# Optimization experiments

Measured on AMD Instinct MI355X. Metric: run time of the kernel, lower is better.

Reference implementation:

```python
import jax, jax.numpy as jnp
import numpy as np

H = 16        # head_nums
DN = 128      # qk_nope_head_dim
DR = 64       # qk_rope_head_dim
DV = 128      # v_head_dim
QLR = 1536    # q_lora_rank
KVLR = 512    # kv_lora_rank
HID = 2048    # hidden_dim
THETA = 10000.0
EPS = 1e-6


def _rms(x, w):
    return x * jax.lax.rsqrt(jnp.mean(x * x, axis=-1, keepdims=True) + EPS) * w


def _reorder(x):
    # replicates view(b,h,s,d//2,2).transpose(4,3).reshape: [x0,x2,...,x1,x3,...]
    return jnp.concatenate([x[..., 0::2], x[..., 1::2]], axis=-1)


def _rotate_half(x):
    h = x.shape[-1] // 2
    return jnp.concatenate([-x[..., h:], x[..., :h]], axis=-1)


def setup_inputs() -> dict:
    key = jax.random.key(0)
    ks = jax.random.split(key, 7)
    B, S = 1, 2048

    def w(k, i, o):
        return jax.random.normal(k, (i, o), jnp.float32) * (i ** -0.5)

    return {
        "x": jax.random.normal(ks[0], (B, S, HID), jnp.float32),
        "Wq_down": w(ks[1], HID, QLR),
        "q_norm_w": jnp.ones((QLR,), jnp.float32),
        "Wq_up": w(ks[2], QLR, H * (DN + DR)),
        "Wkv_down": w(ks[3], HID, KVLR + DR),
        "kv_norm_w": jnp.ones((KVLR,), jnp.float32),
        "Wkv_up": w(ks[4], KVLR, H * (DN + DV)),
        "Wo": w(ks[5], HID, HID),
        "position": jnp.broadcast_to(jnp.arange(S, dtype=jnp.int32)[None], (B, S)),
        "mask": jnp.tril(jnp.ones((S, S), bool))[None, None],  # causal [1,1,S,S]
    }


def reference(x, Wq_down, q_norm_w, Wq_up, Wkv_down, kv_norm_w, Wkv_up, Wo, position, mask):
    B, S, _ = x.shape
    # low-rank Q path: down-proj -> RMSNorm -> up-proj -> [B,H,S,DN+DR]
    q = _rms(x @ Wq_down, q_norm_w) @ Wq_up
    q = q.reshape(B, S, H, DN + DR).transpose(0, 2, 1, 3)
    q_nope, q_rope = q[..., :DN], q[..., DN:]
    # latent KV path
    ckv = x @ Wkv_down
    c, k_rope = ckv[..., :KVLR], ckv[..., KVLR:]
    c = _rms(c, kv_norm_w)
    kv = (c @ Wkv_up).reshape(B, S, H, DN + DV).transpose(0, 2, 1, 3)
    k_nope, v = kv[..., :DN], kv[..., DN:]
    k_rope = k_rope[:, None]  # [B,1,S,DR] shared across heads
    # rotary tables
    inv_freq = 1.0 / (THETA ** (jnp.arange(0, DR, 2, dtype=jnp.float32) / DR))
    t = jnp.arange(S, dtype=jnp.float32)
    emb = jnp.concatenate([jnp.outer(t, inv_freq)] * 2, axis=-1)  # [S,DR]
    cos = jnp.cos(emb)[position][:, None]  # [B,1,S,DR]
    sin = jnp.sin(emb)[position][:, None]
    qr, kr = _reorder(q_rope), _reorder(k_rope)
    q_rot = qr * cos + _rotate_half(qr) * sin
    k_rot = kr * cos + _rotate_half(kr) * sin
    q_state = jnp.concatenate([q_nope, q_rot], axis=-1)              # [B,H,S,DN+DR]
    k_state = jnp.concatenate(
        [k_nope, jnp.broadcast_to(k_rot, (B, H, S, DR))], axis=-1)   # [B,H,S,DN+DR]
    scores = jnp.einsum('bhsd,bhtd->bhst', q_state, k_state) / np.float32(np.sqrt(DV))
    scores = jnp.where(mask, scores, -jnp.inf)
    att = jax.nn.softmax(scores, axis=-1)
    out = jnp.einsum('bhst,bhtd->bhsd', att, v)
    out = out.transpose(0, 2, 1, 3).reshape(B, S, H * DV)
    return out @ Wo
```

## Files before the change

kernel.cpp:

```cpp
#include <hip/hip_runtime.h>
#include <hip/hip_bf16.h>
#include <cstddef>

#define H 16
#define DN 128
#define DR 64
#define DV 128
#define QLR 1536
#define KVLR 512
#define HID 2048
#define SLEN 2048
#define EPS 1e-6f
#define SCALE 0.08838834764831845f
#define QK_SCALE (0.08838834764831845f * 1.4426950408889634f)

typedef __attribute__((ext_vector_type(8))) short short8;
typedef __attribute__((ext_vector_type(4))) float f32x4;
typedef unsigned short u16;

__device__ __forceinline__ u16 f2bf(float f) {
    __hip_bfloat16 h = __float2bfloat16(f);
    return __builtin_bit_cast(u16, h);
}
__device__ __forceinline__ float b2f(u16 v) {
    return __bfloat162float(__builtin_bit_cast(__hip_bfloat16, v));
}
__device__ __forceinline__ unsigned pack2(float a, float b) {
    return (unsigned)f2bf(a) | ((unsigned)f2bf(b) << 16);
}

__global__ __launch_bounds__(256) void prep_all(
    const float* __restrict__ x, u16* __restrict__ xb,
    const float* __restrict__ Wqd, const float* __restrict__ Wkvd,
    const float* __restrict__ Wqu, const float* __restrict__ Wkvu,
    const float* __restrict__ Wo,
    u16* __restrict__ BtF, u16* __restrict__ Wqu_t,
    u16* __restrict__ Wkvu_t, u16* __restrict__ Wo_t)
{
    const int tid = threadIdx.x;
    if (blockIdx.x < 2048) {
        size_t base = ((size_t)blockIdx.x * 256 + tid) * 8;
        float4 v0 = *reinterpret_cast<const float4*>(x + base);
        float4 v1 = *reinterpret_cast<const float4*>(x + base + 4);
        union { short8 s; unsigned u[4]; } p;
        p.u[0] = pack2(v0.x, v0.y); p.u[1] = pack2(v0.z, v0.w);
        p.u[2] = pack2(v1.x, v1.y); p.u[3] = pack2(v1.z, v1.w);
        *reinterpret_cast<short8*>(xb + base) = p.s;
        return;
    }
    int b = blockIdx.x - 2048;
    const float* W; u16* Wt; int K, N, nx; float scale = 1.0f;
    if (b < 768)       { W = Wqd;  Wt = BtF;                          K = 2048; N = 1536; nx = 24; }
    else if (b < 1088) { b -= 768;  W = Wkvd; Wt = BtF + (size_t)1536 * 2048; K = 2048; N = 576;  nx = 10; }
    else if (b < 2240) { b -= 1088; W = Wqu;  Wt = Wqu_t;             K = 1536; N = 3072; nx = 48; scale = QK_SCALE; }
    else if (b < 2752) { b -= 2240; W = Wkvu; Wt = Wkvu_t;            K = 512;  N = 4096; nx = 64; }
    else               { b -= 2752; W = Wo;   Wt = Wo_t;              K = 2048; N = 2048; nx = 32; }
    const int bx = b % nx, by = b / nx;

    __shared__ float T[64][65];
    const int n0 = bx * 64, k0 = by * 64;
    const bool inb = (n0 < N);
    {
        int r = tid >> 4, c4 = (tid & 15) * 4;
        #pragma unroll
        for (int rr = 0; rr < 4; ++rr) {
            int row = rr * 16 + r;
            float4 v = inb ? *reinterpret_cast<const float4*>(W + (size_t)(k0 + row) * N + n0 + c4)
                           : make_float4(0.f, 0.f, 0.f, 0.f);
            T[row][c4] = v.x * scale; T[row][c4 + 1] = v.y * scale;
            T[row][c4 + 2] = v.z * scale; T[row][c4 + 3] = v.w * scale;
        }
    }
    __syncthreads();
    {
        int n = tid >> 2, kq = (tid & 3) * 16;
        unsigned u[8];
        #pragma unroll
        for (int jj = 0; jj < 8; ++jj)
            u[jj] = pack2(T[kq + 2 * jj][n], T[kq + 2 * jj + 1][n]);
        u16* dst = Wt + (size_t)(n0 + n) * K + k0 + kq;
        *reinterpret_cast<uint4*>(dst)     = make_uint4(u[0], u[1], u[2], u[3]);
        *reinterpret_cast<uint4*>(dst + 8) = make_uint4(u[4], u[5], u[6], u[7]);
    }
}

__device__ __forceinline__ void stage4(const char* Gb, const unsigned* srcOff,
                                       const int* ldsBase, u16* smemBuf, unsigned koff)
{
    #pragma unroll
    for (int j = 0; j < 4; ++j)
        __builtin_amdgcn_global_load_lds(
            (const __attribute__((address_space(1))) unsigned int*)(Gb + srcOff[j] + koff),
            (__attribute__((address_space(3))) unsigned int*)(smemBuf + ldsBase[j]),
            16, 0, 0);
}

template<bool BF16OUT>
__global__ __launch_bounds__(256) void gemm_bf16(
    const u16* __restrict__ A, const u16* __restrict__ Bt,
    void* __restrict__ Cv, int M, int N, int K)
{
    __shared__ u16 smem[2][8192];
    const int tid = threadIdx.x, lane = tid & 63, w = tid >> 6;

    const int nbx = gridDim.x, nby = gridDim.y;
    const int nwg = nbx * nby;
    int orig = blockIdx.y * nbx + blockIdx.x;
    int xcd = orig & 7, o8 = orig >> 3;
    int qq = nwg >> 3, rr = nwg & 7;
    int v = (xcd < rr ? xcd * (qq + 1) : rr * (qq + 1) + (xcd - rr) * qq) + o8;
    int bx = v / nby, by = v - bx * nby;
    const int m0 = by * 128, n0 = bx * 128;
    const size_t Kb = (size_t)K * 2;

    unsigned srcOff[4];
    int ldsBase[4];
    #pragma unroll
    for (int j = 0; j < 4; ++j) {
        int c = w * 4 + j;
        int o = (c & 7) * 1024 + lane * 16;
        int u = o ^ (((o >> 7) & 3) << 4);
        int row = u >> 6, kbyte = u & 63;
        srcOff[j] = (unsigned)((size_t)((c < 8 ? m0 : n0) + row) * Kb + kbyte);
        ldsBase[j] = (c < 8) ? (c * 512) : (4096 + (c - 8) * 512);
    }
    const char* Gb = (w < 2) ? (const char*)A : (const char*)Bt;

    const int wr = (w >> 1) * 64, wc = (w & 1) * 64;
    int aoff[4], boff[4];
    #pragma unroll
    for (int i = 0; i < 4; ++i) {
        int oa = (wr + i * 16 + (lane & 15)) * 64 + (lane >> 4) * 16;
        aoff[i] = oa ^ (((oa >> 7) & 3) << 4);
        int ob = (wc + i * 16 + (lane & 15)) * 64 + (lane >> 4) * 16;
        boff[i] = (ob ^ (((ob >> 7) & 3) << 4)) + 8192;
    }

    f32x4 acc[4][4];
    #pragma unroll
    for (int i = 0; i < 4; ++i)
        #pragma unroll
        for (int j = 0; j < 4; ++j) acc[i][j] = (f32x4){0.f, 0.f, 0.f, 0.f};

    const int NT = K >> 5;
    stage4(Gb, srcOff, ldsBase, &smem[0][0], 0);
    __syncthreads();
    int cur = 0;
    for (int t = 0; t < NT; ++t) {
        if (t + 1 < NT) stage4(Gb, srcOff, ldsBase, &smem[cur ^ 1][0], (unsigned)(t + 1) * 64);
        const char* base = (const char*)&smem[cur][0];
        short8 af[4], bfr[4];
        #pragma unroll
        for (int i = 0; i < 4; ++i) af[i] = *reinterpret_cast<const short8*>(base + aoff[i]);
        #pragma unroll
        for (int i = 0; i < 4; ++i) bfr[i] = *reinterpret_cast<const short8*>(base + boff[i]);
        __builtin_amdgcn_s_setprio(1);
        #pragma unroll
        for (int i = 0; i < 4; ++i)
            #pragma unroll
            for (int j = 0; j < 4; ++j)
                acc[i][j] = __builtin_amdgcn_mfma_f32_16x16x32_bf16(af[i], bfr[j], acc[i][j], 0, 0, 0);
        __builtin_amdgcn_s_setprio(0);
        __syncthreads();
        cur ^= 1;
    }

    #pragma unroll
    for (int i = 0; i < 4; ++i) {
        int grow0 = m0 + wr + i * 16 + ((lane >> 4) * 4);
        #pragma unroll
        for (int j = 0; j < 4; ++j) {
            int gcol = n0 + wc + j * 16 + (lane & 15);
            if (gcol < N) {
                #pragma unroll
                for (int r = 0; r < 4; ++r) {
                    float v2 = acc[i][j][r];
                    if (BF16OUT) ((u16*)Cv)[(size_t)(grow0 + r) * N + gcol] = f2bf(v2);
                    else         ((float*)Cv)[(size_t)(grow0 + r) * N + gcol] = v2;
                }
            }
        }
    }
}

__global__ __launch_bounds__(256) void rmsnorm2_bf16(
    const float* __restrict__ fC, const float* __restrict__ qw,
    const float* __restrict__ kvw, u16* __restrict__ qdb, u16* __restrict__ ckvb)
{
    const int row = blockIdx.x, tid = threadIdx.x;
    const float* p = fC + (size_t)row * 2112;
    float ssq = 0.f, ssk = 0.f;
    for (int i = tid * 4; i < 1536; i += 1024) {
        float4 v = *reinterpret_cast<const float4*>(p + i);
        ssq += v.x * v.x + v.y * v.y + v.z * v.z + v.w * v.w;
    }
    if (tid < 128) {
        float4 v = *reinterpret_cast<const float4*>(p + 1536 + tid * 4);
        ssk = v.x * v.x + v.y * v.y + v.z * v.z + v.w * v.w;
    }
    __shared__ float wsq[4], wsk[4];
    int lane = tid & 63, wv = tid >> 6;
    #pragma unroll
    for (int off = 32; off; off >>= 1) {
        ssq += __shfl_down(ssq, off);
        ssk += __shfl_down(ssk, off);
    }
    if (lane == 0) { wsq[wv] = ssq; wsk[wv] = ssk; }
    __syncthreads();
    if (tid == 0) {
        wsq[0] = rsqrtf((wsq[0] + wsq[1] + wsq[2] + wsq[3]) / 1536.f + EPS);
        wsk[0] = rsqrtf((wsk[0] + wsk[1] + wsk[2] + wsk[3]) / 512.f + EPS);
    }
    __syncthreads();
    float scq = wsq[0], sck = wsk[0];
    for (int i = tid * 4; i < 1536; i += 1024) {
        float4 v = *reinterpret_cast<const float4*>(p + i);
        float4 g = *reinterpret_cast<const float4*>(qw + i);
        *reinterpret_cast<uint2*>(qdb + (size_t)row * 1536 + i) =
            make_uint2(pack2(v.x * scq * g.x, v.y * scq * g.y),
                       pack2(v.z * scq * g.z, v.w * scq * g.w));
    }
    if (tid < 128) {
        int i = tid * 4;
        float4 v = *reinterpret_cast<const float4*>(p + 1536 + i);
        float4 g = *reinterpret_cast<const float4*>(kvw + i);
        *reinterpret_cast<uint2*>(ckvb + (size_t)row * 512 + i) =
            make_uint2(pack2(v.x * sck * g.x, v.y * sck * g.y),
                       pack2(v.z * sck * g.z, v.w * sck * g.w));
    }
}

__global__ __launch_bounds__(256) void rope_bf16(
    u16* __restrict__ q, const float* __restrict__ krsrc, int krStride,
    u16* __restrict__ krot)
{
    const int s = blockIdx.x, tid = threadIdx.x;
    __shared__ float cs[32], sn[32];
    if (tid < 32) {
        float inv = powf(10000.0f, -(float)tid / 32.0f);
        float ang = (float)s * inv;
        cs[tid] = cosf(ang); sn[tid] = sinf(ang);
    }
    __syncthreads();
    float ev[2], ov[2]; int hh[2], ii[2];
    #pragma unroll
    for (int it = 0; it < 2; ++it) {
        int pidx = tid + it * 256;
        int h = pidx >> 5, i = pidx & 31;
        hh[it] = h; ii[it] = i;
        const u16* base = q + (size_t)s * 3072 + h * 192 + 128;
        ev[it] = b2f(base[2 * i]); ov[it] = b2f(base[2 * i + 1]);
    }
    __syncthreads();
    #pragma unroll
    for (int it = 0; it < 2; ++it) {
        int h = hh[it], i = ii[it];
        u16* base = q + (size_t)s * 3072 + h * 192 + 128;
        base[i]      = f2bf(ev[it] * cs[i] - ov[it] * sn[i]);
        base[32 + i] = f2bf(ov[it] * cs[i] + ev[it] * sn[i]);
    }
    if (tid < 32) {
        int i = tid;
        float e = krsrc[(size_t)s * krStride + 2 * i];
        float o = krsrc[(size_t)s * krStride + 2 * i + 1];
        krot[(size_t)s * 64 + i]      = f2bf(e * cs[i] - o * sn[i]);
        krot[(size_t)s * 64 + 32 + i] = f2bf(o * cs[i] + e * sn[i]);
    }
}

__global__ __launch_bounds__(256, 2) void attn_chunk(
    const u16* __restrict__ qbf,
    const u16* __restrict__ kvbf,
    const u16* __restrict__ krot,
    u16* __restrict__ outb,
    u16* __restrict__ partAcc,
    float* __restrict__ partML)
{
    const int bid = blockIdx.x;
    const int xcd = bid & 7, slot = bid >> 3;
    const int h = xcd + 8 * (slot & 1);
    const int r80 = 79 - (slot >> 1);
    int qb, ch, S, poff;
    if (r80 < 8)       { qb = r80;                 ch = 0;      S = 1; poff = 0; }
    else if (r80 < 24) { int u = r80 - 8;  qb = 8 + (u >> 1);  ch = u & 1; S = 2; poff = (qb - 8) * 2 + ch; }
    else if (r80 < 48) { int u = r80 - 24; qb = 16 + u / 3;    ch = u % 3; S = 3; poff = 16 + (qb - 16) * 3 + ch; }
    else               { int u = r80 - 48; qb = 24 + (u >> 2); ch = u & 3; S = 4; poff = 40 + (qb - 24) * 4 + ch; }
    const int s0 = qb * 64;
    const int t0 = ch * 8;
    const int t1 = (t0 + 8 < qb + 1) ? (t0 + 8) : (qb + 1);
    const int slotId = h * 72 + poff;
    const int tid = threadIdx.x, lane = tid & 63, w = tid >> 6;
    const int colk = lane & 15, grp = lane >> 4, g8 = grp * 8;

    __shared__ u16 Ks[64 * 192];
    __shared__ u16 Vt[128 * 64];
    __shared__ u16 Ps[64 * 64];

    short8 qreg[6];
    {
        const u16* qp = qbf + ((size_t)(s0 + w * 16 + colk) * H + h) * 192;
        #pragma unroll
        for (int ks = 0; ks < 6; ++ks)
            qreg[ks] = *reinterpret_cast<const short8*>(qp + ks * 32 + g8);
    }

    int kt[6], kslot[6];
    #pragma unroll
    for (int it = 0; it < 6; ++it) {
        int c = it * 256 + tid;
        kt[it] = c / 24; kslot[it] = c % 24;
    }
    int vd2[2], vt8[2];
    #pragma unroll
    for (int it = 0; it < 2; ++it) {
        int c = it * 256 + tid;
        vd2[it] = c & 63; vt8[it] = c >> 6;
    }

    short8 kreg[6];
    unsigned vreg[2][8];

    auto issue_loads = [&](int t) {
        #pragma unroll
        for (int it = 0; it < 6; ++it) {
            int gk = t * 64 + kt[it];
            const u16* src = (kslot[it] < 16)
                ? kvbf + ((size_t)gk * H + h) * 256 + kslot[it] * 8
                : krot + (size_t)gk * 64 + (kslot[it] - 16) * 8;
            kreg[it] = *reinterpret_cast<const short8*>(src);
        }
        #pragma unroll
        for (int it = 0; it < 2; ++it)
            #pragma unroll
            for (int j = 0; j < 8; ++j)
                vreg[it][j] = *reinterpret_cast<const unsigned*>(
                    kvbf + ((size_t)(t * 64 + vt8[it] * 8 + j) * H + h) * 256 + 128 + 2 * vd2[it]);
    };
    auto write_lds = [&]() {
        #pragma unroll
        for (int it = 0; it < 6; ++it) {
            int sl = (kslot[it] & 24) | ((kslot[it] ^ kt[it]) & 7);
            *reinterpret_cast<short8*>(&Ks[kt[it] * 192 + sl * 8]) = kreg[it];
        }
        #pragma unroll
        for (int it = 0; it < 2; ++it) {
            uint4 lo, hi;
            unsigned* lp = &lo.x; unsigned* hp = &hi.x;
            #pragma unroll
            for (int p2 = 0; p2 < 4; ++p2) {
                unsigned a = vreg[it][2 * p2], b = vreg[it][2 * p2 + 1];
                lp[p2] = (a & 0xffffu) | (b << 16);
                hp[p2] = (a >> 16) | (b & 0xffff0000u);
            }
            int sl = (vt8[it] ^ vd2[it]) & 7;
            *reinterpret_cast<uint4*>(&Vt[vd2[it] * 64 + sl * 8]) = lo;
            *reinterpret_cast<uint4*>(&Vt[(64 + vd2[it]) * 64 + sl * 8]) = hi;
        }
    };

    float m_run[4] = {-1e30f, -1e30f, -1e30f, -1e30f};
    float l_run[4] = {0.f, 0.f, 0.f, 0.f};
    f32x4 acc_o[8];
    #pragma unroll
    for (int i = 0; i < 8; ++i) acc_o[i] = (f32x4){0.f, 0.f, 0.f, 0.f};

    issue_loads(t0);
    for (int t = t0; t < t1; ++t) {
        __syncthreads();
        write_lds();
        __syncthreads();
        if (t + 1 < t1) issue_loads(t + 1);

        f32x4 sacc[4];
        #pragma unroll
        for (int ct = 0; ct < 4; ++ct) sacc[ct] = (f32x4){0.f, 0.f, 0.f, 0.f};
        __builtin_amdgcn_s_setprio(1);
        #pragma unroll
        for (int ks = 0; ks < 6; ++ks) {
            #pragma unroll
            for (int ct = 0; ct < 4; ++ct) {
                int key = ct * 16 + colk;
                int slotIdx = ks * 4 + grp;
                int sl = (slotIdx & 24) | ((slotIdx ^ key) & 7);
                short8 b = *reinterpret_cast<const short8*>(&Ks[key * 192 + sl * 8]);
                sacc[ct] = __builtin_amdgcn_mfma_f32_16x16x32_bf16(qreg[ks], b, sacc[ct], 0, 0, 0);
            }
        }
        __builtin_amdgcn_s_setprio(0);

        const bool lastTile = (t == qb);
        float sv[4][4], lmax[4];
        bool need = false;
        #pragma unroll
        for (int r = 0; r < 4; ++r) {
            int qg = s0 + w * 16 + grp * 4 + r;
            #pragma unroll
            for (int ct = 0; ct < 4; ++ct) {
                float val = sacc[ct][r];
                if (lastTile) {
                    int key = t * 64 + ct * 16 + colk;
                    val = (key <= qg) ? val : -1e30f;
                }
                sv[r][ct] = val;
            }
            lmax[r] = fmaxf(fmaxf(sv[r][0], sv[r][1]), fmaxf(sv[r][2], sv[r][3]));
            need = need || (lmax[r] > m_run[r] + 11.5f);
        }
        if (__any((int)need)) {
            #pragma unroll
            for (int r = 0; r < 4; ++r) {
                float m = lmax[r];
                m = fmaxf(m, __shfl_xor(m, 1));
                m = fmaxf(m, __shfl_xor(m, 2));
                m = fmaxf(m, __shfl_xor(m, 4));
                m = fmaxf(m, __shfl_xor(m, 8));
                float mnew = fmaxf(m_run[r], m);
                float f = exp2f(m_run[r] - mnew);
                m_run[r] = mnew;
                l_run[r] *= f;
                #pragma unroll
                for (int ct = 0; ct < 8; ++ct) acc_o[ct][r] *= f;
            }
        }
        #pragma unroll
        for (int r = 0; r < 4; ++r) {
            int prow = w * 16 + grp * 4 + r;
            float psum = 0.f;
            #pragma unroll
            for (int ct = 0; ct < 4; ++ct) {
                float pz = exp2f(sv[r][ct] - m_run[r]);
                int col = ct * 16 + colk;
                Ps[prow * 64 + ((((col >> 3) ^ prow) & 7) << 3) + (col & 7)] = f2bf(pz);
                psum += pz;
            }
            l_run[r] += psum;
        }

        __builtin_amdgcn_s_setprio(1);
        #pragma unroll
        for (int ks2 = 0; ks2 < 2; ++ks2) {
            int prow = w * 16 + colk;
            int psl = ((ks2 * 4 + grp) ^ prow) & 7;
            short8 pa = *reinterpret_cast<const short8*>(&Ps[prow * 64 + psl * 8]);
            #pragma unroll
            for (int ct = 0; ct < 8; ++ct) {
                int cc = ct * 16 + colk;
                int phys = (cc >> 1) + (cc & 1) * 64;
                int vsl = ((ks2 * 4 + grp) ^ phys) & 7;
                short8 vb = *reinterpret_cast<const short8*>(&Vt[phys * 64 + vsl * 8]);
                acc_o[ct] = __builtin_amdgcn_mfma_f32_16x16x32_bf16(pa, vb, acc_o[ct], 0, 0, 0);
            }
        }
        __builtin_amdgcn_s_setprio(0);
    }

    #pragma unroll
    for (int r = 0; r < 4; ++r) {
        float l = l_run[r];
        l += __shfl_xor(l, 1);
        l += __shfl_xor(l, 2);
        l += __shfl_xor(l, 4);
        l += __shfl_xor(l, 8);
        int rloc = w * 16 + grp * 4 + r;
        int grow = s0 + rloc;
        if (S == 1) {
            float invl = 1.0f / l;
            #pragma unroll
            for (int ct = 0; ct < 8; ++ct)
                outb[(size_t)grow * 2048 + h * 128 + ct * 16 + colk] = f2bf(acc_o[ct][r] * invl);
        } else {
            if (colk == 0) {
                partML[(size_t)slotId * 128 + rloc * 2]     = m_run[r];
                partML[(size_t)slotId * 128 + rloc * 2 + 1] = l;
            }
            u16* pa = partAcc + (size_t)slotId * 8192 + rloc * 128;
            #pragma unroll
            for (int ct = 0; ct < 8; ++ct)
                pa[ct * 16 + colk] = f2bf(acc_o[ct][r]);
        }
    }
}

__global__ __launch_bounds__(256) void attn_combine(
    const u16* __restrict__ partAcc, const float* __restrict__ partML,
    u16* __restrict__ outb)
{
    const int bid = blockIdx.x;
    const int xcd = bid & 7, s2 = bid >> 3;
    const int h = xcd + 8 * (s2 / 24);
    const int qb = 8 + s2 % 24;
    int S, poff;
    if (qb < 16)      { S = 2; poff = (qb - 8) * 2; }
    else if (qb < 24) { S = 3; poff = 16 + (qb - 16) * 3; }
    else              { S = 4; poff = 40 + (qb - 24) * 4; }
    const int base = h * 72 + poff;
    const int tid = threadIdx.x;
    const int row = tid >> 2, seg = (tid & 3) * 32;

    float mv[4], lv[4];
    float m_g = -1e30f;
    #pragma unroll
    for (int s = 0; s < 4; ++s) {
        bool ok = (s < S);
        mv[s] = ok ? partML[(size_t)(base + s) * 128 + row * 2]     : -1e30f;
        lv[s] = ok ? partML[(size_t)(base + s) * 128 + row * 2 + 1] : 0.f;
        m_g = fmaxf(m_g, mv[s]);
    }
    float l_g = 0.f, wq[4];
    #pragma unroll
    for (int s = 0; s < 4; ++s) { wq[s] = exp2f(mv[s] - m_g); l_g += wq[s] * lv[s]; }
    float inv = 1.f / l_g;
    u16* orow = outb + (size_t)(qb * 64 + row) * 2048 + h * 128 + seg;
    #pragma unroll
    for (int i = 0; i < 8; ++i) {
        float o[4] = {0.f, 0.f, 0.f, 0.f};
        #pragma unroll
        for (int s = 0; s < 4; ++s) {
            if (s < S) {
                ushort4 a = *reinterpret_cast<const ushort4*>(
                    partAcc + (size_t)(base + s) * 8192 + row * 128 + seg + i * 4);
                o[0] += wq[s] * b2f(a.x); o[1] += wq[s] * b2f(a.y);
                o[2] += wq[s] * b2f(a.z); o[3] += wq[s] * b2f(a.w);
            }
        }
        uint2 pk;
        pk.x = pack2(o[0] * inv, o[1] * inv);
        pk.y = pack2(o[2] * inv, o[3] * inv);
        *reinterpret_cast<uint2*>(orow + i * 4) = pk;
    }
}

extern "C" void kernel_launch(void* const* d_in, const int* in_sizes, int n_in,
                              void* d_out, int out_size, void* d_ws, size_t ws_size,
                              hipStream_t stream)
{
    (void)in_sizes; (void)n_in; (void)out_size; (void)ws_size;
    const float* x         = (const float*)d_in[0];
    const float* Wq_down   = (const float*)d_in[1];
    const float* q_norm_w  = (const float*)d_in[2];
    const float* Wq_up     = (const float*)d_in[3];
    const float* Wkv_down  = (const float*)d_in[4];
    const float* kv_norm_w = (const float*)d_in[5];
    const float* Wkv_up    = (const float*)d_in[6];
    const float* Wo        = (const float*)d_in[7];
    float* out = (float*)d_out;

    char* p = (char*)d_ws;
    u16* BtF     = (u16*)p;   p += (size_t)2176 * 2048 * 2;
    u16* Wkvu_t  = (u16*)p;   p += (size_t)4096 * 512  * 2;
    u16* Wo_t    = (u16*)p;   p += (size_t)2048 * 2048 * 2;
    u16* qbuf    = (u16*)p;   p += (size_t)2048 * 3072 * 2;
    u16* ckvb    = (u16*)p;   p += (size_t)2048 * 512  * 2;
    u16* kvbf    = (u16*)p;   p += (size_t)2048 * 4096 * 2;
    u16* krotb   = (u16*)p;   p += (size_t)2048 * 64   * 2;
    u16* xb      = (u16*)p;   p += (size_t)2048 * 2048 * 2;
    u16* Wqu_t   = (u16*)p;   p += (size_t)3072 * 1536 * 2;
    float* fC    = (float*)p; p += (size_t)2048 * 2112 * 4;
    u16* qdb     = (u16*)p;   p += (size_t)2048 * 1536 * 2;
    u16* attb    = (u16*)BtF;
    u16* partAcc = xb;
    float* partML  = (float*)(partAcc + (size_t)1152 * 8192);

    dim3 blk(256);
    prep_all<<<5824, blk, 0, stream>>>(x, xb, Wq_down, Wkv_down, Wq_up, Wkv_up, Wo,
                                       BtF, Wqu_t, Wkvu_t, Wo_t);

    gemm_bf16<false><<<dim3(17, 16), blk, 0, stream>>>(xb, BtF, fC, 2048, 2112, 2048);
    rmsnorm2_bf16<<<2048, blk, 0, stream>>>(fC, q_norm_w, kv_norm_w, qdb, ckvb);
    gemm_bf16<true><<<dim3(24, 16), blk, 0, stream>>>(qdb, Wqu_t, qbuf, 2048, 3072, 1536);
    gemm_bf16<true><<<dim3(32, 16), blk, 0, stream>>>(ckvb, Wkvu_t, kvbf, 2048, 4096, 512);
    rope_bf16<<<2048, blk, 0, stream>>>(qbuf, fC + 2048, 2112, krotb);

    attn_chunk<<<dim3(1280), blk, 0, stream>>>(qbuf, kvbf, krotb, attb, partAcc, partML);
    attn_combine<<<dim3(384), blk, 0, stream>>>(partAcc, partML, attb);

    gemm_bf16<false><<<dim3(16, 16), blk, 0, stream>>>(attb, Wo_t, out, 2048, 2048, 2048);
}
```

Measured before the change: 221.3 us.

## Transpose attention MFMAs to keep P in registers instead of LDS

Swaps the MFMA operand order so the score tile comes out transposed, with each lane owning one query row. Masking, row max and row sum then run per lane with fewer cross-lane shuffles. The P tile is passed to the PV matmul through register shuffles rather than a shared-memory round trip, which removes the Ps buffer. Outputs are stored as packed 4-element vectors. The cost is extra shuffle and select instructions per tile, and the lane remapping carries correctness risk.

New measurement: 217.3 us. Within noise of the previous version (-1.8%).

```diff
diff --git a/kernel.cpp b/kernel.cpp
--- a/kernel.cpp
+++ b/kernel.cpp
@@ -294,11 +294,12 @@
 
     __shared__ u16 Ks[64 * 192];
     __shared__ u16 Vt[128 * 64];
-    __shared__ u16 Ps[64 * 64];
+
+    const int qg = s0 + w * 16 + colk;
 
     short8 qreg[6];
     {
-        const u16* qp = qbf + ((size_t)(s0 + w * 16 + colk) * H + h) * 192;
+        const u16* qp = qbf + ((size_t)qg * H + h) * 192;
         #pragma unroll
         for (int ks = 0; ks < 6; ++ks)
             qreg[ks] = *reinterpret_cast<const short8*>(qp + ks * 32 + g8);
@@ -358,11 +359,14 @@
         }
     };
 
-    float m_run[4] = {-1e30f, -1e30f, -1e30f, -1e30f};
-    float l_run[4] = {0.f, 0.f, 0.f, 0.f};
+    float m_run = -1e30f, l_run = 0.f;
     f32x4 acc_o[8];
     #pragma unroll
     for (int i = 0; i < 8; ++i) acc_o[i] = (f32x4){0.f, 0.f, 0.f, 0.f};
+
+    const int srcA = colk + ((grp & 1) << 5);
+    const int srcB = srcA + 16;
+    const bool hiSel = (grp >> 1) != 0;
 
     issue_loads(t0);
     for (int t = t0; t < t1; ++t) {
@@ -382,101 +386,110 @@
                 int key = ct * 16 + colk;
                 int slotIdx = ks * 4 + grp;
                 int sl = (slotIdx & 24) | ((slotIdx ^ key) & 7);
-                short8 b = *reinterpret_cast<const short8*>(&Ks[key * 192 + sl * 8]);
-                sacc[ct] = __builtin_amdgcn_mfma_f32_16x16x32_bf16(qreg[ks], b, sacc[ct], 0, 0, 0);
+                short8 kf = *reinterpret_cast<const short8*>(&Ks[key * 192 + sl * 8]);
+                sacc[ct] = __builtin_amdgcn_mfma_f32_16x16x32_bf16(kf, qreg[ks], sacc[ct], 0, 0, 0);
             }
         }
         __builtin_amdgcn_s_setprio(0);
 
-        const bool lastTile = (t == qb);
-        float sv[4][4], lmax[4];
-        bool need = false;
-        #pragma unroll
-        for (int r = 0; r < 4; ++r) {
-            int qg = s0 + w * 16 + grp * 4 + r;
+        if (t == qb) {
             #pragma unroll
             for (int ct = 0; ct < 4; ++ct) {
-                float val = sacc[ct][r];
-                if (lastTile) {
-                    int key = t * 64 + ct * 16 + colk;
-                    val = (key <= qg) ? val : -1e30f;
-                }
-                sv[r][ct] = val;
-            }
-            lmax[r] = fmaxf(fmaxf(sv[r][0], sv[r][1]), fmaxf(sv[r][2], sv[r][3]));
-            need = need || (lmax[r] > m_run[r] + 11.5f);
-        }
+                int keyb = t * 64 + ct * 16 + 4 * grp;
+                #pragma unroll
+                for (int r = 0; r < 4; ++r)
+                    if (keyb + r > qg) sacc[ct][r] = -1e30f;
+            }
+        }
+
+        float lmax = fmaxf(fmaxf(fmaxf(sacc[0][0], sacc[0][1]), fmaxf(sacc[0][2], sacc[0][3])),
+                           fmaxf(fmaxf(sacc[1][0], sacc[1][1]), fmaxf(sacc[1][2], sacc[1][3])));
+        lmax = fmaxf(lmax,
+               fmaxf(fmaxf(fmaxf(sacc[2][0], sacc[2][1]), fmaxf(sacc[2][2], sacc[2][3])),
+                     fmaxf(fmaxf(sacc[3][0], sacc[3][1]), fmaxf(sacc[3][2], sacc[3][3]))));
+        bool need = lmax > m_run + 11.5f;
         if (__any((int)need)) {
-            #pragma unroll
-            for (int r = 0; r < 4; ++r) {
-                float m = lmax[r];
-                m = fmaxf(m, __shfl_xor(m, 1));
-                m = fmaxf(m, __shfl_xor(m, 2));
-                m = fmaxf(m, __shfl_xor(m, 4));
-                m = fmaxf(m, __shfl_xor(m, 8));
-                float mnew = fmaxf(m_run[r], m);
-                float f = exp2f(m_run[r] - mnew);
-                m_run[r] = mnew;
-                l_run[r] *= f;
-                #pragma unroll
-                for (int ct = 0; ct < 8; ++ct) acc_o[ct][r] *= f;
-            }
-        }
-        #pragma unroll
-        for (int r = 0; r < 4; ++r) {
-            int prow = w * 16 + grp * 4 + r;
-            float psum = 0.f;
-            #pragma unroll
-            for (int ct = 0; ct < 4; ++ct) {
-                float pz = exp2f(sv[r][ct] - m_run[r]);
-                int col = ct * 16 + colk;
-                Ps[prow * 64 + ((((col >> 3) ^ prow) & 7) << 3) + (col & 7)] = f2bf(pz);
-                psum += pz;
-            }
-            l_run[r] += psum;
-        }
+            float mx = fmaxf(m_run, lmax);
+            mx = fmaxf(mx, __shfl_xor(mx, 16));
+            mx = fmaxf(mx, __shfl_xor(mx, 32));
+            float f = exp2f(m_run - mx);
+            m_run = mx;
+            l_run *= f;
+            #pragma unroll
+            for (int i = 0; i < 8; ++i) {
+                acc_o[i][0] *= f; acc_o[i][1] *= f;
+                acc_o[i][2] *= f; acc_o[i][3] *= f;
+            }
+        }
+
+        unsigned pku[8];
+        float psum = 0.f;
+        #pragma unroll
+        for (int ct = 0; ct < 4; ++ct) {
+            float p0 = exp2f(sacc[ct][0] - m_run);
+            float p1 = exp2f(sacc[ct][1] - m_run);
+            float p2 = exp2f(sacc[ct][2] - m_run);
+            float p3 = exp2f(sacc[ct][3] - m_run);
+            psum += (p0 + p1) + (p2 + p3);
+            pku[ct * 2]     = pack2(p0, p1);
+            pku[ct * 2 + 1] = pack2(p2, p3);
+        }
+        l_run += psum;
 
         __builtin_amdgcn_s_setprio(1);
         #pragma unroll
         for (int ks2 = 0; ks2 < 2; ++ks2) {
-            int prow = w * 16 + colk;
-            int psl = ((ks2 * 4 + grp) ^ prow) & 7;
-            short8 pa = *reinterpret_cast<const short8*>(&Ps[prow * 64 + psl * 8]);
+            unsigned a0 = __shfl(pku[4 * ks2 + 0], srcA);
+            unsigned a1 = __shfl(pku[4 * ks2 + 1], srcA);
+            unsigned a2 = __shfl(pku[4 * ks2 + 0], srcB);
+            unsigned a3 = __shfl(pku[4 * ks2 + 1], srcB);
+            unsigned b0 = __shfl(pku[4 * ks2 + 2], srcA);
+            unsigned b1 = __shfl(pku[4 * ks2 + 3], srcA);
+            unsigned b2 = __shfl(pku[4 * ks2 + 2], srcB);
+            unsigned b3 = __shfl(pku[4 * ks2 + 3], srcB);
+            union { short8 s; unsigned u[4]; } bq;
+            bq.u[0] = hiSel ? b0 : a0;
+            bq.u[1] = hiSel ? b1 : a1;
+            bq.u[2] = hiSel ? b2 : a2;
+            bq.u[3] = hiSel ? b3 : a3;
             #pragma unroll
             for (int ct = 0; ct < 8; ++ct) {
                 int cc = ct * 16 + colk;
                 int phys = (cc >> 1) + (cc & 1) * 64;
                 int vsl = ((ks2 * 4 + grp) ^ phys) & 7;
                 short8 vb = *reinterpret_cast<const short8*>(&Vt[phys * 64 + vsl * 8]);
-                acc_o[ct] = __builtin_amdgcn_mfma_f32_16x16x32_bf16(pa, vb, acc_o[ct], 0, 0, 0);
+                acc_o[ct] = __builtin_amdgcn_mfma_f32_16x16x32_bf16(vb, bq.s, acc_o[ct], 0, 0, 0);
             }
         }
         __builtin_amdgcn_s_setprio(0);
     }
 
-    #pragma unroll
-    for (int r = 0; r < 4; ++r) {
-        float l = l_run[r];
-        l += __shfl_xor(l, 1);
-        l += __shfl_xor(l, 2);
-        l += __shfl_xor(l, 4);
-        l += __shfl_xor(l, 8);
-        int rloc = w * 16 + grp * 4 + r;
-        int grow = s0 + rloc;
-        if (S == 1) {
-            float invl = 1.0f / l;
-            #pragma unroll
-            for (int ct = 0; ct < 8; ++ct)
-                outb[(size_t)grow * 2048 + h * 128 + ct * 16 + colk] = f2bf(acc_o[ct][r] * invl);
-        } else {
-            if (colk == 0) {
-                partML[(size_t)slotId * 128 + rloc * 2]     = m_run[r];
-                partML[(size_t)slotId * 128 + rloc * 2 + 1] = l;
-            }
-            u16* pa = partAcc + (size_t)slotId * 8192 + rloc * 128;
-            #pragma unroll
-            for (int ct = 0; ct < 8; ++ct)
-                pa[ct * 16 + colk] = f2bf(acc_o[ct][r]);
+    float l = l_run;
+    l += __shfl_xor(l, 16);
+    l += __shfl_xor(l, 32);
+    const int rloc = w * 16 + colk;
+    if (S == 1) {
+        float invl = 1.0f / l;
+        u16* orow = outb + (size_t)qg * 2048 + h * 128 + 4 * grp;
+        #pragma unroll
+        for (int ct = 0; ct < 8; ++ct) {
+            uint2 pk;
+            pk.x = pack2(acc_o[ct][0] * invl, acc_o[ct][1] * invl);
+            pk.y = pack2(acc_o[ct][2] * invl, acc_o[ct][3] * invl);
+            *reinterpret_cast<uint2*>(orow + ct * 16) = pk;
+        }
+    } else {
+        if (grp == 0) {
+            partML[(size_t)slotId * 128 + rloc * 2]     = m_run;
+            partML[(size_t)slotId * 128 + rloc * 2 + 1] = l;
+        }
+        u16* pa = partAcc + (size_t)slotId * 8192 + rloc * 128 + 4 * grp;
+        #pragma unroll
+        for (int ct = 0; ct < 8; ++ct) {
+            uint2 pk;
+            pk.x = pack2(acc_o[ct][0], acc_o[ct][1]);
+            pk.y = pack2(acc_o[ct][2], acc_o[ct][3]);
+            *reinterpret_cast<uint2*>(pa + ct * 16) = pk;
         }
     }
 }
```
